# Kernel tuning notes

Measured on AMD Instinct MI355X. Metric: run time of the kernel, lower is better.

The kernel has to match this reference:

```python
import jax, jax.numpy as jnp
import numpy as np

N, F, H, E = 20000, 512, 8, 320000
D = F // H
SCALING = D ** (-0.5)


def _layernorm(x, g, b, eps=1e-5):
    mu = jnp.mean(x, axis=-1, keepdims=True)
    var = jnp.var(x, axis=-1, keepdims=True)
    return (x - mu) * jax.lax.rsqrt(var + eps) * g + b


def setup_inputs() -> dict:
    key = jax.random.key(0)
    ks = jax.random.split(key, 12)
    feat = jax.random.normal(ks[0], (N, F), dtype=jnp.float32)
    edge_src = jax.random.randint(ks[1], (E,), 0, N, dtype=jnp.int32)
    edge_dst = jax.random.randint(ks[2], (E,), 0, N, dtype=jnp.int32)
    # self-loops on the first N edges so every node has in-degree >= 1
    loops = jnp.arange(N, dtype=jnp.int32)
    edge_src = edge_src.at[:N].set(loops)
    edge_dst = edge_dst.at[:N].set(loops)
    s = 1.0 / np.sqrt(F)
    def w(k, shape, scale=s):
        return jax.random.normal(k, shape, dtype=jnp.float32) * scale
    return {
        "feat": feat, "edge_src": edge_src, "edge_dst": edge_dst,
        "Wq": w(ks[3], (F, F)), "Wk": w(ks[4], (F, F)), "Wv": w(ks[5], (F, F)),
        "Wnode": w(ks[6], (F, F)), "Wskip": w(ks[7], (F, F)),
        "Wgate": w(ks[8], (3 * F, 1), scale=1.0 / np.sqrt(3 * F)),
        "ln1_g": jnp.ones((F,), jnp.float32), "ln1_b": jnp.zeros((F,), jnp.float32),
        "ln2_g": jnp.ones((F,), jnp.float32), "ln2_b": jnp.zeros((F,), jnp.float32),
        "W1": w(ks[9], (F, F)), "W2": w(ks[10], (F, F)),
    }


def reference(feat, edge_src, edge_dst, Wq, Wk, Wv, Wnode, Wskip, Wgate,
              ln1_g, ln1_b, ln2_g, ln2_b, W1, W2):
    # --- attention (GraphMultiAttentionV2, use_efeats=False, eval mode) ---
    q = (feat @ Wq).reshape(N, H, D)
    k = (feat @ Wk).reshape(N, H, D)
    v = (feat @ Wv).reshape(N, H, D)
    # u_dot_v: per-edge per-head dot product  [E, H]
    logits = jnp.einsum('ehd,ehd->eh', q[edge_src], k[edge_dst])
    logits = jnp.clip(logits, -5.0, 5.0) / SCALING  # faithful: a / scaling
    # edge softmax grouped by destination node
    m = jax.ops.segment_max(logits, edge_dst, num_segments=N)  # [N, H]
    ex = jnp.exp(logits - m[edge_dst])
    denom = jax.ops.segment_sum(ex, edge_dst, num_segments=N)
    sa = ex / denom[edge_dst]  # [E, H]
    # u_mul_e + sum aggregation
    msg = v[edge_src] * sa[..., None]  # [E, H, D]
    agg = jax.ops.segment_sum(msg, edge_dst, num_segments=N).reshape(N, F)
    rst = agg @ Wnode
    # --- gated residual ---
    skip = feat @ Wskip
    gate = jax.nn.sigmoid(jnp.concatenate([rst, skip, rst - skip], axis=-1) @ Wgate)
    h = _layernorm(rst * gate + skip * (1.0 - gate), ln1_g, ln1_b)
    # --- FFN + residual ---
    ffn = jax.nn.relu(_layernorm(h, ln2_g, ln2_b) @ W1) @ W2
    return h + ffn
```

## Files before the change

### kernel.cpp

```cpp
#include <hip/hip_runtime.h>
#include <hip/hip_bf16.h>
#include <hip/hip_fp16.h>

#define NN 20000
#define FD 512
#define NH 8
#define NE 320000
#define MP 20096

typedef unsigned int u32;
typedef unsigned short u16;
typedef __bf16 bf16x8 __attribute__((ext_vector_type(8)));
typedef _Float16 f16x8 __attribute__((ext_vector_type(8)));
typedef float f32x4 __attribute__((ext_vector_type(4)));

#define AS1 __attribute__((address_space(1)))
#define AS3 __attribute__((address_space(3)))

__device__ __forceinline__ u16 f2bf(float f) {
  __hip_bfloat16 h = __float2bfloat16(f);
  union { __hip_bfloat16 b; u16 u; } c; c.b = h; return c.u;
}
__device__ __forceinline__ float bf2f(u32 u) { return __uint_as_float(u << 16); }
__device__ __forceinline__ u16 f2h(float f) {
  union { __half h; u16 u; } c; c.h = __float2half(f); return c.u;
}
__device__ __forceinline__ void gl_lds16(const void* g, void* l) {
  __builtin_amdgcn_global_load_lds((AS1 void*)const_cast<void*>(g), (AS3 void*)l, 16, 0, 0);
}
__device__ __forceinline__ void up_h4(uint2 w, float* f) {
  union { u32 u; __half2 h; } c;
  c.u = w.x; float2 t0 = __half22float2(c.h); f[0]=t0.x; f[1]=t0.y;
  c.u = w.y; float2 t1 = __half22float2(c.h); f[2]=t1.x; f[3]=t1.y;
}

__global__ __launch_bounds__(256) void k_wprep(const float* __restrict__ feat,
    const float* __restrict__ Wq, const float* __restrict__ Wk,
    const float* __restrict__ Wv, const float* __restrict__ Wsk,
    const float* __restrict__ Wn, const float* __restrict__ W1,
    const float* __restrict__ W2, const float* __restrict__ Wg,
    u16* __restrict__ Af, u16* __restrict__ Bqkvs, u16* __restrict__ Bnt,
    u16* __restrict__ B1t, u16* __restrict__ B2t,
    float* __restrict__ gA, float* __restrict__ gB)
{
  int idx = blockIdx.x * 256 + threadIdx.x;
  if (idx < MP * FD / 4) {
    size_t i = (size_t)idx * 4;
    float4 v = make_float4(0.f, 0.f, 0.f, 0.f);
    if (i < (size_t)NN * FD) v = *(const float4*)(feat + i);
    *(ushort4*)(Af + i) = make_ushort4(f2h(v.x), f2h(v.y), f2h(v.z), f2h(v.w));
    return;
  }
  idx -= MP * FD / 4;
  if (idx < 2048 * 512) {
    int n = idx >> 9, k = idx & 511;
    float v;
    if (n < 512)       v = Wq[k * 512 + n];
    else if (n < 1024) v = Wk[k * 512 + (n - 512)];
    else if (n < 1536) v = Wv[k * 512 + (n - 1024)];
    else               v = Wsk[k * 512 + (n - 1536)];
    Bqkvs[idx] = f2h(v);
    return;
  }
  idx -= 2048 * 512;
  if (idx < 512 * 512) { int n = idx >> 9, k = idx & 511; Bnt[idx] = f2bf(Wn[k * 512 + n]); return; }
  idx -= 512 * 512;
  if (idx < 512 * 512) { int n = idx >> 9, k = idx & 511; B1t[idx] = f2bf(W1[k * 512 + n]); return; }
  idx -= 512 * 512;
  if (idx < 512 * 512) { int n = idx >> 9, k = idx & 511; B2t[idx] = f2bf(W2[k * 512 + n]); return; }
  idx -= 512 * 512;
  if (idx < 512) {
    gA[idx] = Wg[idx] + Wg[2 * 512 + idx];
    gB[idx] = Wg[512 + idx] - Wg[2 * 512 + idx];
  }
}

template<int NCOLS, int MODE, int FP16>
__global__ __launch_bounds__(256, 4) void k_gemm(
    const u16* __restrict__ A, const u16* __restrict__ B,
    float* __restrict__ Cf, u16* __restrict__ Cb, u16* __restrict__ Cb2,
    u16* __restrict__ Cb3, int Mreal)
{
  const long brow = (long)blockIdx.x * 128;
  if (brow >= MP) return;
  __shared__ u16 sA[2][128 * 32];
  __shared__ u16 sB[2][128 * 32];
  const int tid = threadIdx.x, lane = tid & 63, w = tid >> 6;
  const int wr = w >> 1, wc = w & 1;
  const long bcol = (long)blockIdx.y * 128;
  const int srl = tid >> 2, scl = (tid & 3) * 8;

  auto stage = [&](int b, int kt) {
#pragma unroll
    for (int s = 0; s < 2; s++) {
      gl_lds16(A + (brow + s * 64 + srl) * FD + kt + scl, &sA[b][s * 2048 + w * 512]);
      gl_lds16(B + (bcol + s * 64 + srl) * FD + kt + scl, &sB[b][s * 2048 + w * 512]);
    }
  };

  f32x4 acc[4][4] = {};
  stage(0, 0);
  __syncthreads();
  int cur = 0;
  const int ro = (lane >> 4) * 8;
  for (int kt = 0; kt < FD; kt += 32) {
    if (kt + 32 < FD) stage(cur ^ 1, kt + 32);
#pragma unroll
    for (int m = 0; m < 4; m++) {
      const u16* pa = &sA[cur][(wr * 64 + m * 16 + (lane & 15)) * 32 + ro];
#pragma unroll
      for (int n = 0; n < 4; n++) {
        const u16* pb = &sB[cur][(wc * 64 + n * 16 + (lane & 15)) * 32 + ro];
        if constexpr (FP16)
          acc[m][n] = __builtin_amdgcn_mfma_f32_16x16x32_f16(
              *(const f16x8*)pa, *(const f16x8*)pb, acc[m][n], 0, 0, 0);
        else
          acc[m][n] = __builtin_amdgcn_mfma_f32_16x16x32_bf16(
              *(const bf16x8*)pa, *(const bf16x8*)pb, acc[m][n], 0, 0, 0);
      }
    }
    __syncthreads();
    cur ^= 1;
  }
#pragma unroll
  for (int m = 0; m < 4; m++) {
    long row0 = brow + wr * 64 + m * 16 + (lane >> 4) * 4;
#pragma unroll
    for (int n = 0; n < 4; n++) {
      long col = bcol + wc * 64 + n * 16 + (lane & 15);
#pragma unroll
      for (int j = 0; j < 4; j++) {
        long row = row0 + j;
        if (row < Mreal) {
          float v = acc[m][n][j];
          if constexpr (MODE == 1) Cb[row * NCOLS + col] = f2bf(fmaxf(v, 0.f));
          else if constexpr (MODE == 2) Cb[row * NCOLS + col] = f2bf(v);
          else if constexpr (MODE == 3) Cf[row * NCOLS + col] += v;
          else {
            if (col < 512)       Cb[row * 1024 + col] = f2h(v);
            else if (col < 1024) Cb2[row * 512 + (col - 512)] = f2h(v);
            else if (col < 1536) Cb[row * 1024 + 512 + (col - 1024)] = f2h(v);
            else                 Cb3[row * 512 + (col - 1536)] = f2bf(v);
          }
        }
      }
    }
  }
}

__global__ __launch_bounds__(256) void k_deg(const int* __restrict__ dst, int* __restrict__ deg)
{
  int e = blockIdx.x * 256 + threadIdx.x;
  if (e < NE) atomicAdd(&deg[dst[e]], 1);
}

__global__ void k_scan(const int* __restrict__ deg, int* __restrict__ offa)
{
  __shared__ int wsum[16];
  __shared__ int carry;
  const int tid = threadIdx.x, lane = tid & 63, wid = tid >> 6;
  if (tid == 0) { carry = 0; offa[0] = 0; }
  __syncthreads();
  for (int base = 0; base < NN; base += 1024) {
    int i = base + tid;
    int s = (i < NN) ? deg[i] : 0;
#pragma unroll
    for (int d = 1; d < 64; d <<= 1) {
      int t = __shfl_up(s, d);
      if (lane >= d) s += t;
    }
    if (lane == 63) wsum[wid] = s;
    __syncthreads();
    if (tid < 16) {
      int ws = wsum[tid];
#pragma unroll
      for (int d = 1; d < 16; d <<= 1) {
        int t = __shfl_up(ws, d, 16);
        if (tid >= d) ws += t;
      }
      wsum[tid] = ws;
    }
    __syncthreads();
    int add = carry + (wid ? wsum[wid - 1] : 0);
    if (i < NN) offa[i + 1] = add + s;
    __syncthreads();
    if (tid == 0) carry += wsum[15];
    __syncthreads();
  }
}

__global__ __launch_bounds__(256) void k_scatter(const int* __restrict__ src, const int* __restrict__ dst,
    const int* __restrict__ offa, int* __restrict__ cnt, int* __restrict__ esrcs)
{
  int e = blockIdx.x * 256 + threadIdx.x;
  if (e >= NE) return;
  int d = dst[e];
  int p = offa[d] + atomicAdd(&cnt[d], 1);
  esrcs[p] = src[e];
}

__global__ __launch_bounds__(256) void k_edge(const int* __restrict__ offa,
    const int* __restrict__ esrcs, const u16* __restrict__ QV,
    const u16* __restrict__ Kb, u16* __restrict__ aggb)
{
  int wid = blockIdx.x * 4 + (threadIdx.x >> 6);
  int nd = wid >> 1, half = wid & 1;
  int lane = threadIdx.x & 63;
  if (nd >= MP) return;
  const int off = half * 256 + lane * 4;
  u16* op = aggb + (size_t)nd * FD + off;
  if (nd >= NN) { *(ushort4*)op = make_ushort4(0, 0, 0, 0); return; }
  uint2 kw = *(const uint2*)(Kb + (size_t)nd * 512 + off);
  float kx[4]; up_h4(kw, kx);
  int b0 = offa[nd], b1 = offa[nd + 1];
  float den = 0.f, a0 = 0.f, a1 = 0.f, a2 = 0.f, a3 = 0.f;
  for (int p = b0; p < b1; p += 8) {
    int ss[8]; uint2 qw[8], vw[8];
#pragma unroll
    for (int u = 0; u < 8; u++) { int ix = p + u; ss[u] = esrcs[ix < b1 ? ix : b1 - 1]; }
#pragma unroll
    for (int u = 0; u < 8; u++) {
      const u16* r = QV + (size_t)ss[u] * 1024 + off;
      qw[u] = *(const uint2*)r;
      vw[u] = *(const uint2*)(r + 512);
    }
#pragma unroll
    for (int u = 0; u < 8; u++) {
      float qx[4]; up_h4(qw[u], qx);
      float d = qx[0]*kx[0] + qx[1]*kx[1] + qx[2]*kx[2] + qx[3]*kx[3];
      d += __shfl_xor(d, 1); d += __shfl_xor(d, 2);
      d += __shfl_xor(d, 4); d += __shfl_xor(d, 8);
      float ex = __expf(fminf(fmaxf(d, -5.f), 5.f) * 8.f - 40.f);
      ex = (p + u < b1) ? ex : 0.f;
      den += ex;
      float vx[4]; up_h4(vw[u], vx);
      a0 += ex * vx[0]; a1 += ex * vx[1]; a2 += ex * vx[2]; a3 += ex * vx[3];
    }
  }
  float rd = 1.f / den;
  *(ushort4*)op = make_ushort4(f2bf(a0*rd), f2bf(a1*rd), f2bf(a2*rd), f2bf(a3*rd));
}

__device__ __forceinline__ float blkred(float v, float* sb)
{
#pragma unroll
  for (int s = 1; s < 64; s <<= 1) v += __shfl_xor(v, s);
  __syncthreads();
  if ((threadIdx.x & 63) == 0) sb[threadIdx.x >> 6] = v;
  __syncthreads();
  return sb[0] + sb[1];
}

__global__ __launch_bounds__(128) void k_gate_ln(const u16* __restrict__ rstb, const u16* __restrict__ skpb,
    const float* __restrict__ gA, const float* __restrict__ gB,
    const float* __restrict__ g1, const float* __restrict__ b1,
    const float* __restrict__ g2, const float* __restrict__ b2,
    float* __restrict__ hout, u16* __restrict__ h2b)
{
  __shared__ float sb[2];
  const int t = threadIdx.x;
  const size_t base = (size_t)blockIdx.x * FD + t * 4;
  ushort4 ru = *(const ushort4*)(rstb + base);
  ushort4 su = *(const ushort4*)(skpb + base);
  float r0 = bf2f(ru.x), r1 = bf2f(ru.y), r2 = bf2f(ru.z), r3 = bf2f(ru.w);
  float s0 = bf2f(su.x), s1 = bf2f(su.y), s2 = bf2f(su.z), s3 = bf2f(su.w);
  float4 av = *(const float4*)(gA + t * 4);
  float4 bv = *(const float4*)(gB + t * 4);
  float gd = r0*av.x + r1*av.y + r2*av.z + r3*av.w
           + s0*bv.x + s1*bv.y + s2*bv.z + s3*bv.w;
  float tot = blkred(gd, sb);
  float g = 1.f / (1.f + __expf(-tot));
  float x0 = g*r0 + (1.f-g)*s0;
  float x1 = g*r1 + (1.f-g)*s1;
  float x2 = g*r2 + (1.f-g)*s2;
  float x3 = g*r3 + (1.f-g)*s3;
  float m1 = blkred(x0+x1+x2+x3, sb) * (1.f/FD);
  float d0 = x0-m1, d1 = x1-m1, d2 = x2-m1, d3 = x3-m1;
  float v1 = blkred(d0*d0+d1*d1+d2*d2+d3*d3, sb) * (1.f/FD);
  float rs = rsqrtf(v1 + 1e-5f);
  float4 G1 = *(const float4*)(g1 + t*4);
  float4 Bb1 = *(const float4*)(b1 + t*4);
  float h0 = d0*rs*G1.x + Bb1.x;
  float h1 = d1*rs*G1.y + Bb1.y;
  float h2 = d2*rs*G1.z + Bb1.z;
  float h3 = d3*rs*G1.w + Bb1.w;
  *(float4*)(hout + base) = make_float4(h0, h1, h2, h3);
  float m2 = blkred(h0+h1+h2+h3, sb) * (1.f/FD);
  float e0 = h0-m2, e1 = h1-m2, e2 = h2-m2, e3 = h3-m2;
  float v2 = blkred(e0*e0+e1*e1+e2*e2+e3*e3, sb) * (1.f/FD);
  float rs2 = rsqrtf(v2 + 1e-5f);
  float4 G2 = *(const float4*)(g2 + t*4);
  float4 Bb2 = *(const float4*)(b2 + t*4);
  *(ushort4*)(h2b + base) = make_ushort4(
      f2bf(e0*rs2*G2.x + Bb2.x), f2bf(e1*rs2*G2.y + Bb2.y),
      f2bf(e2*rs2*G2.z + Bb2.z), f2bf(e3*rs2*G2.w + Bb2.w));
}

extern "C" void kernel_launch(void* const* d_in, const int* in_sizes, int n_in,
                              void* d_out, int out_size, void* d_ws, size_t ws_size,
                              hipStream_t stream)
{
  const float* feat = (const float*)d_in[0];
  const int* e_src = (const int*)d_in[1];
  const int* e_dst = (const int*)d_in[2];
  const float* Wq  = (const float*)d_in[3];
  const float* Wk  = (const float*)d_in[4];
  const float* Wv  = (const float*)d_in[5];
  const float* Wn  = (const float*)d_in[6];
  const float* Wsk = (const float*)d_in[7];
  const float* Wg  = (const float*)d_in[8];
  const float* l1g = (const float*)d_in[9];
  const float* l1b = (const float*)d_in[10];
  const float* l2g = (const float*)d_in[11];
  const float* l2b = (const float*)d_in[12];
  const float* W1  = (const float*)d_in[13];
  const float* W2  = (const float*)d_in[14];

  char* ws = (char*)d_ws;
  size_t o = 0;
  auto al = [&](size_t b) { char* r = ws + o; o = (o + b + 255) & ~(size_t)255; return r; };

  u16* Af    = (u16*)al((size_t)MP * FD * 2);
  u16* Bqkvs = (u16*)al((size_t)2048 * FD * 2);
  u16* Bnt   = (u16*)al((size_t)FD * FD * 2);
  u16* B1t   = (u16*)al((size_t)FD * FD * 2);
  u16* B2t   = (u16*)al((size_t)FD * FD * 2);
  float* gA  = (float*)al(FD * 4);
  float* gB  = (float*)al(FD * 4);
  u16* QV    = (u16*)al((size_t)MP * 1024 * 2);
  u16* Kb    = (u16*)al((size_t)MP * FD * 2);
  u16* SKIPb = (u16*)al((size_t)MP * FD * 2);
  u16* aggb  = (u16*)al((size_t)MP * FD * 2);
  u16* h2b   = (u16*)al((size_t)MP * FD * 2);
  int* deg   = (int*)al((size_t)2 * NN * 4);
  int* cnt   = deg + NN;
  int* offa  = (int*)al((size_t)(NN + 1) * 4);
  int* esrcs = (int*)al((size_t)NE * 4);
  if (o > ws_size) return;
  u16* rstb = Kb;
  u16* midb = Af;
  float* out = (float*)d_out;

  hipMemsetAsync(deg, 0, (size_t)2 * NN * 4, stream);

  {
    int total = MP * FD / 4 + 2048 * 512 + 3 * 512 * 512 + 512;
    k_wprep<<<dim3((total + 255) / 256), 256, 0, stream>>>(feat, Wq, Wk, Wv, Wsk, Wn, W1, W2, Wg,
        Af, Bqkvs, Bnt, B1t, B2t, gA, gB);
  }

  k_gemm<2048, 6, 1><<<dim3(160, 16), 256, 0, stream>>>(Af, Bqkvs, nullptr, QV, Kb, SKIPb, MP);

  k_deg<<<dim3((NE + 255) / 256), 256, 0, stream>>>(e_dst, deg);
  k_scan<<<dim3(1), 1024, 0, stream>>>(deg, offa);
  k_scatter<<<dim3((NE + 255) / 256), 256, 0, stream>>>(e_src, e_dst, offa, cnt, esrcs);
  k_edge<<<dim3(MP / 2), 256, 0, stream>>>(offa, esrcs, QV, Kb, aggb);

  k_gemm<512, 2, 0><<<dim3(160, 4), 256, 0, stream>>>(aggb, Bnt, nullptr, rstb, nullptr, nullptr, MP);
  k_gate_ln<<<dim3(NN), 128, 0, stream>>>(rstb, SKIPb, gA, gB, l1g, l1b, l2g, l2b, out, h2b);
  k_gemm<512, 1, 0><<<dim3(160, 4), 256, 0, stream>>>(h2b, B1t, nullptr, midb, nullptr, nullptr, MP);
  k_gemm<512, 3, 0><<<dim3(160, 4), 256, 0, stream>>>(midb, B2t, out, nullptr, nullptr, nullptr, NN);
}
```

Before: 330.7 us.

## Widen QKV GEMM tile, fuse degree count, single-pass scan, bf16 residual

The QKV/skip GEMM now uses a 128x256 tile, so the A tile is reused across twice as many columns, with fewer blocks and three blocks per CU. The degree-count atomics are folded into the weight-prep kernel, which removes one launch. The scan now does a single pass in which each thread handles 20 elements. The gated-LN output h is written in bf16 and added in the final GEMM epilogue, replacing an fp32 write followed by a read-modify-write. The residual h is rounded to bf16, which costs accuracy, and the wider tile raises register pressure.

```diff
diff --git a/kernel.cpp b/kernel.cpp
--- a/kernel.cpp
+++ b/kernel.cpp
@@ -39,9 +39,10 @@
     const float* __restrict__ Wv, const float* __restrict__ Wsk,
     const float* __restrict__ Wn, const float* __restrict__ W1,
     const float* __restrict__ W2, const float* __restrict__ Wg,
+    const int* __restrict__ e_dst,
     u16* __restrict__ Af, u16* __restrict__ Bqkvs, u16* __restrict__ Bnt,
     u16* __restrict__ B1t, u16* __restrict__ B2t,
-    float* __restrict__ gA, float* __restrict__ gB)
+    float* __restrict__ gA, float* __restrict__ gB, int* __restrict__ deg)
 {
   int idx = blockIdx.x * 256 + threadIdx.x;
   if (idx < MP * FD / 4) {
@@ -72,33 +73,38 @@
   if (idx < 512) {
     gA[idx] = Wg[idx] + Wg[2 * 512 + idx];
     gB[idx] = Wg[512 + idx] - Wg[2 * 512 + idx];
-  }
-}
-
-template<int NCOLS, int MODE, int FP16>
-__global__ __launch_bounds__(256, 4) void k_gemm(
+    return;
+  }
+  idx -= 512;
+  if (idx < NE) atomicAdd(&deg[e_dst[idx]], 1);
+}
+
+template<int NCOLS, int MODE, int FP16, int BN>
+__global__ __launch_bounds__(256, (BN == 256) ? 3 : 4) void k_gemm(
     const u16* __restrict__ A, const u16* __restrict__ B,
     float* __restrict__ Cf, u16* __restrict__ Cb, u16* __restrict__ Cb2,
     u16* __restrict__ Cb3, int Mreal)
 {
+  constexpr int NF = BN / 32;
   const long brow = (long)blockIdx.x * 128;
   if (brow >= MP) return;
   __shared__ u16 sA[2][128 * 32];
-  __shared__ u16 sB[2][128 * 32];
+  __shared__ u16 sB[2][BN * 32];
   const int tid = threadIdx.x, lane = tid & 63, w = tid >> 6;
   const int wr = w >> 1, wc = w & 1;
-  const long bcol = (long)blockIdx.y * 128;
+  const long bcol = (long)blockIdx.y * BN;
   const int srl = tid >> 2, scl = (tid & 3) * 8;
 
   auto stage = [&](int b, int kt) {
 #pragma unroll
-    for (int s = 0; s < 2; s++) {
+    for (int s = 0; s < 2; s++)
       gl_lds16(A + (brow + s * 64 + srl) * FD + kt + scl, &sA[b][s * 2048 + w * 512]);
+#pragma unroll
+    for (int s = 0; s < BN / 64; s++)
       gl_lds16(B + (bcol + s * 64 + srl) * FD + kt + scl, &sB[b][s * 2048 + w * 512]);
-    }
   };
 
-  f32x4 acc[4][4] = {};
+  f32x4 acc[4][NF] = {};
   stage(0, 0);
   __syncthreads();
   int cur = 0;
@@ -109,8 +115,8 @@
     for (int m = 0; m < 4; m++) {
       const u16* pa = &sA[cur][(wr * 64 + m * 16 + (lane & 15)) * 32 + ro];
 #pragma unroll
-      for (int n = 0; n < 4; n++) {
-        const u16* pb = &sB[cur][(wc * 64 + n * 16 + (lane & 15)) * 32 + ro];
+      for (int n = 0; n < NF; n++) {
+        const u16* pb = &sB[cur][(wc * (BN / 2) + n * 16 + (lane & 15)) * 32 + ro];
         if constexpr (FP16)
           acc[m][n] = __builtin_amdgcn_mfma_f32_16x16x32_f16(
               *(const f16x8*)pa, *(const f16x8*)pb, acc[m][n], 0, 0, 0);
@@ -126,8 +132,8 @@
   for (int m = 0; m < 4; m++) {
     long row0 = brow + wr * 64 + m * 16 + (lane >> 4) * 4;
 #pragma unroll
-    for (int n = 0; n < 4; n++) {
-      long col = bcol + wc * 64 + n * 16 + (lane & 15);
+    for (int n = 0; n < NF; n++) {
+      long col = bcol + wc * (BN / 2) + n * 16 + (lane & 15);
 #pragma unroll
       for (int j = 0; j < 4; j++) {
         long row = row0 + j;
@@ -135,12 +141,14 @@
           float v = acc[m][n][j];
           if constexpr (MODE == 1) Cb[row * NCOLS + col] = f2bf(fmaxf(v, 0.f));
           else if constexpr (MODE == 2) Cb[row * NCOLS + col] = f2bf(v);
-          else if constexpr (MODE == 3) Cf[row * NCOLS + col] += v;
-          else {
+          else if constexpr (MODE == 6) {
             if (col < 512)       Cb[row * 1024 + col] = f2h(v);
             else if (col < 1024) Cb2[row * 512 + (col - 512)] = f2h(v);
             else if (col < 1536) Cb[row * 1024 + 512 + (col - 1024)] = f2h(v);
             else                 Cb3[row * 512 + (col - 1536)] = f2bf(v);
+          } else {
+            long o = row * NCOLS + col;
+            Cf[o] = bf2f((u32)Cb2[o]) + v;
           }
         }
       }
@@ -148,44 +156,37 @@
   }
 }
 
-__global__ __launch_bounds__(256) void k_deg(const int* __restrict__ dst, int* __restrict__ deg)
-{
-  int e = blockIdx.x * 256 + threadIdx.x;
-  if (e < NE) atomicAdd(&deg[dst[e]], 1);
-}
-
-__global__ void k_scan(const int* __restrict__ deg, int* __restrict__ offa)
+__global__ __launch_bounds__(1024) void k_scan(const int* __restrict__ deg, int* __restrict__ offa)
 {
   __shared__ int wsum[16];
-  __shared__ int carry;
   const int tid = threadIdx.x, lane = tid & 63, wid = tid >> 6;
-  if (tid == 0) { carry = 0; offa[0] = 0; }
-  __syncthreads();
-  for (int base = 0; base < NN; base += 1024) {
-    int i = base + tid;
-    int s = (i < NN) ? deg[i] : 0;
-#pragma unroll
-    for (int d = 1; d < 64; d <<= 1) {
-      int t = __shfl_up(s, d);
-      if (lane >= d) s += t;
-    }
-    if (lane == 63) wsum[wid] = s;
-    __syncthreads();
-    if (tid < 16) {
-      int ws = wsum[tid];
-#pragma unroll
-      for (int d = 1; d < 16; d <<= 1) {
-        int t = __shfl_up(ws, d, 16);
-        if (tid >= d) ws += t;
-      }
-      wsum[tid] = ws;
-    }
-    __syncthreads();
-    int add = carry + (wid ? wsum[wid - 1] : 0);
-    if (i < NN) offa[i + 1] = add + s;
-    __syncthreads();
-    if (tid == 0) carry += wsum[15];
-    __syncthreads();
+  const int base = tid * 20;
+  int loc[20];
+  int s = 0;
+#pragma unroll
+  for (int j = 0; j < 20; j++) {
+    int i = base + j;
+    int v = (i < NN) ? deg[i] : 0;
+    s += v; loc[j] = s;
+  }
+  int incl = s;
+#pragma unroll
+  for (int d = 1; d < 64; d <<= 1) { int t = __shfl_up(incl, d); if (lane >= d) incl += t; }
+  if (lane == 63) wsum[wid] = incl;
+  __syncthreads();
+  if (tid < 16) {
+    int ws = wsum[tid];
+#pragma unroll
+    for (int d = 1; d < 16; d <<= 1) { int t = __shfl_up(ws, d, 16); if (tid >= d) ws += t; }
+    wsum[tid] = ws;
+  }
+  __syncthreads();
+  int prev = incl - s + (wid ? wsum[wid - 1] : 0);
+  if (tid == 0) offa[0] = 0;
+#pragma unroll
+  for (int j = 0; j < 20; j++) {
+    int i = base + j;
+    if (i < NN) offa[i + 1] = prev + loc[j];
   }
 }
 
@@ -255,7 +256,7 @@
     const float* __restrict__ gA, const float* __restrict__ gB,
     const float* __restrict__ g1, const float* __restrict__ b1,
     const float* __restrict__ g2, const float* __restrict__ b2,
-    float* __restrict__ hout, u16* __restrict__ h2b)
+    u16* __restrict__ hb, u16* __restrict__ h2b)
 {
   __shared__ float sb[2];
   const int t = threadIdx.x;
@@ -284,7 +285,7 @@
   float h1 = d1*rs*G1.y + Bb1.y;
   float h2 = d2*rs*G1.z + Bb1.z;
   float h3 = d3*rs*G1.w + Bb1.w;
-  *(float4*)(hout + base) = make_float4(h0, h1, h2, h3);
+  *(ushort4*)(hb + base) = make_ushort4(f2bf(h0), f2bf(h1), f2bf(h2), f2bf(h3));
   float m2 = blkred(h0+h1+h2+h3, sb) * (1.f/FD);
   float e0 = h0-m2, e1 = h1-m2, e2 = h2-m2, e3 = h3-m2;
   float v2 = blkred(e0*e0+e1*e1+e2*e2+e3*e3, sb) * (1.f/FD);
@@ -332,6 +333,7 @@
   u16* SKIPb = (u16*)al((size_t)MP * FD * 2);
   u16* aggb  = (u16*)al((size_t)MP * FD * 2);
   u16* h2b   = (u16*)al((size_t)MP * FD * 2);
+  u16* hb    = (u16*)al((size_t)MP * FD * 2);
   int* deg   = (int*)al((size_t)2 * NN * 4);
   int* cnt   = deg + NN;
   int* offa  = (int*)al((size_t)(NN + 1) * 4);
@@ -344,20 +346,19 @@
   hipMemsetAsync(deg, 0, (size_t)2 * NN * 4, stream);
 
   {
-    int total = MP * FD / 4 + 2048 * 512 + 3 * 512 * 512 + 512;
+    int total = MP * FD / 4 + 2048 * 512 + 3 * 512 * 512 + 512 + NE;
     k_wprep<<<dim3((total + 255) / 256), 256, 0, stream>>>(feat, Wq, Wk, Wv, Wsk, Wn, W1, W2, Wg,
-        Af, Bqkvs, Bnt, B1t, B2t, gA, gB);
-  }
-
-  k_gemm<2048, 6, 1><<<dim3(160, 16), 256, 0, stream>>>(Af, Bqkvs, nullptr, QV, Kb, SKIPb, MP);
-
-  k_deg<<<dim3((NE + 255) / 256), 256, 0, stream>>>(e_dst, deg);
+        e_dst, Af, Bqkvs, Bnt, B1t, B2t, gA, gB, deg);
+  }
+
+  k_gemm<2048, 6, 1, 256><<<dim3(160, 8), 256, 0, stream>>>(Af, Bqkvs, nullptr, QV, Kb, SKIPb, MP);
+
   k_scan<<<dim3(1), 1024, 0, stream>>>(deg, offa);
   k_scatter<<<dim3((NE + 255) / 256), 256, 0, stream>>>(e_src, e_dst, offa, cnt, esrcs);
   k_edge<<<dim3(MP / 2), 256, 0, stream>>>(offa, esrcs, QV, Kb, aggb);
 
-  k_gemm<512, 2, 0><<<dim3(160, 4), 256, 0, stream>>>(aggb, Bnt, nullptr, rstb, nullptr, nullptr, MP);
-  k_gate_ln<<<dim3(NN), 128, 0, stream>>>(rstb, SKIPb, gA, gB, l1g, l1b, l2g, l2b, out, h2b);
-  k_gemm<512, 1, 0><<<dim3(160, 4), 256, 0, stream>>>(h2b, B1t, nullptr, midb, nullptr, nullptr, MP);
-  k_gemm<512, 3, 0><<<dim3(160, 4), 256, 0, stream>>>(midb, B2t, out, nullptr, nullptr, nullptr, NN);
-}
+  k_gemm<512, 2, 0, 128><<<dim3(160, 4), 256, 0, stream>>>(aggb, Bnt, nullptr, rstb, nullptr, nullptr, MP);
+  k_gate_ln<<<dim3(NN), 128, 0, stream>>>(rstb, SKIPb, gA, gB, l1g, l1b, l2g, l2b, hb, h2b);
+  k_gemm<512, 1, 0, 128><<<dim3(160, 4), 256, 0, stream>>>(h2b, B1t, nullptr, midb, nullptr, nullptr, NN);
+  k_gemm<512, 7, 0, 128><<<dim3(160, 4), 256, 0, stream>>>(midb, B2t, out, nullptr, hb, nullptr, NN);
+}
```

After: 445.0 us. 1.35x slower.
